# Optimization experiments

Hardware: AMD Instinct MI355X
Metric: run time of the kernel (lower is better)

Reference implementation:

```python
import jax, jax.numpy as jnp
import numpy as np

N, M, D = 16384, 1024, 32


def setup_inputs() -> dict:
    key = jax.random.key(0)
    k1, k2 = jax.random.split(key)
    x = jax.random.normal(k1, (N, D), dtype=jnp.float32)
    centers = jax.random.normal(k2, (M, D), dtype=jnp.float32)
    sigma = jnp.ones((M, D), dtype=jnp.float32)  # get_sigma_ones(s=1.0)
    return {"x": x, "centers": centers, "sigma": sigma}


def reference(x, centers, sigma):
    # Gaussian RBF kernel: exp(-0.5 * delta^T invCov delta) / sqrt((2pi)^D det(S))
    d = x.shape[1]
    s2 = sigma ** 2  # (M, D)
    # invCovMat: inverse of per-center diagonal covariance -> diag(1/s2)
    invCov = jnp.eye(d, dtype=x.dtype) * (1.0 / s2)[:, :, None]  # (M, D, D)
    # denom: sqrt((2pi)^D * prod(s2))
    k = (2.0 * np.pi) ** d  # python float, safe for D=32 in f32
    detS = jnp.sqrt(jnp.asarray(k, x.dtype) * jnp.prod(s2, axis=1))  # (M,)
    delta = x[:, None, :] - centers[None, :, :]  # (N, M, D)
    # batched (1,D) @ (D,D) per (n,m) pair, then elementwise * delta and reduce
    q = jnp.einsum('nmd,mde->nme', delta, invCov)  # (N, M, D)
    X = jnp.sum(q * delta, axis=2)  # (N, M) squared Mahalanobis distance
    return jnp.exp(-0.5 * X) / detS[None, :]  # (N, M)
```

## Files before the change

kernel.cpp:

```cpp
#include <hip/hip_runtime.h>


#define N_  16384
#define M_  1024
#define D_  32
#define NT  32
#define BLK 256

typedef float v4f __attribute__((ext_vector_type(4)));
#define PIN(v) asm volatile("" : "+v"(v))

__global__ __launch_bounds__(BLK, 6) void rbf_kernel(
    const float* __restrict__ x, const float* __restrict__ centers,
    const float* __restrict__ sigma, float* __restrict__ out)
{
    const int tid = threadIdx.x;
    const int m   = blockIdx.x * BLK + tid;
    const int n0  = blockIdx.y * NT;

    __shared__ __align__(16) float r2s[NT];

    {
        const v4f* xg = (const v4f*)(x + (size_t)n0 * D_);
        v4f v = xg[tid];
        float s = fmaf(v.x, v.x, fmaf(v.y, v.y, fmaf(v.z, v.z, v.w * v.w)));
        s += __shfl_xor(s, 1);
        s += __shfl_xor(s, 2);
        s += __shfl_xor(s, 4);
        if ((tid & 7) == 0) r2s[tid >> 3] = s;
    }
    __syncthreads();

    const float L2E      = 1.4426950408889634f;
    const float LOG2_2PI = 2.6514961294723187f;

    float s2_0 = 0.f, ld = 0.f;
    bool uf = true;
    {
        const float* sg = sigma + (size_t)m * D_;
        #pragma unroll
        for (int d = 0; d < D_; ++d) {
            float s  = sg[d];
            float s2 = s * s;
            if (d == 0) s2_0 = s2;
            uf = uf && (s2 == s2_0);
            ld += log2f(s2);
        }
    }

    if (__all((int)uf)) {
        const float w0 = 1.0f / s2_0;
        v4f A[D_ / 4];
        float b = 0.f;
        {
            const v4f* cg = (const v4f*)(centers + (size_t)m * D_);
            #pragma unroll
            for (int j = 0; j < D_ / 4; ++j) {
                v4f c = cg[j];
                v4f a = c * w0;
                A[j] = a;
                b = fmaf(c.x, a.x, b);
                b = fmaf(c.y, a.y, b);
                b = fmaf(c.z, a.z, b);
                b = fmaf(c.w, a.w, b);
            }
        }
        #pragma unroll
        for (int j = 0; j < D_ / 4; ++j) PIN(A[j]);

        const float c0 = fmaf(-0.5f * L2E, b, -0.5f * (D_ * LOG2_2PI + ld));
        const float qc = -0.5f * L2E * w0;

        const v4f* r2v = (const v4f*)r2s;
        float* o0 = out + (size_t)n0 * M_ + m;

        #pragma unroll 1
        for (int i = 0; i < NT; i += 8) {
            v4f ra = r2v[i / 4];
            v4f rb = r2v[i / 4 + 1];
            #pragma unroll
            for (int k = 0; k < 8; ++k) {
                const v4f* row = (const v4f*)(x + (size_t)(n0 + i + k) * D_);
                v4f x0 = row[0], x1 = row[1], x2 = row[2], x3 = row[3];
                v4f x4 = row[4], x5 = row[5], x6 = row[6], x7 = row[7];
                v4f p = x0 * A[0];
                v4f q = x1 * A[1];
                p += x2 * A[2];  q += x3 * A[3];
                p += x4 * A[4];  q += x5 * A[5];
                p += x6 * A[6];  q += x7 * A[7];
                v4f t = p + q;
                float dot = (t.x + t.y) + (t.z + t.w);
                float rr  = (k < 4) ? ra[k] : rb[k - 4];
                float f   = fmaf(L2E, dot, fmaf(qc, rr, c0));
                __builtin_nontemporal_store(__builtin_amdgcn_exp2f(f),
                                            o0 + (size_t)(i + k) * M_);
            }
        }
    } else {
        const float c0 = -0.5f * (D_ * LOG2_2PI + ld);
        const float* cg = centers + (size_t)m * D_;
        const float* sg = sigma   + (size_t)m * D_;
        #pragma unroll 1
        for (int i = 0; i < NT; ++i) {
            const float* xr = x + (size_t)(n0 + i) * D_;
            float a0 = 0.f, a1 = 0.f;
            #pragma unroll
            for (int d = 0; d < D_; d += 2) {
                float s0 = sg[d], s1 = sg[d + 1];
                float t0 = xr[d]     - cg[d];
                float t1 = xr[d + 1] - cg[d + 1];
                a0 = fmaf(t0 * (1.0f / (s0 * s0)), t0, a0);
                a1 = fmaf(t1 * (1.0f / (s1 * s1)), t1, a1);
            }
            float f = fmaf(-0.5f * L2E, a0 + a1, c0);
            out[(size_t)(n0 + i) * M_ + m] = __builtin_amdgcn_exp2f(f);
        }
    }
}

extern "C" void kernel_launch(void* const* d_in, const int* in_sizes, int n_in,
                              void* d_out, int out_size, void* d_ws, size_t ws_size,
                              hipStream_t stream) {
    const float* x = (const float*)d_in[0];
    const float* c = (const float*)d_in[1];
    const float* s = (const float*)d_in[2];
    float* out = (float*)d_out;
    dim3 grid(M_ / BLK, N_ / NT);
    rbf_kernel<<<grid, BLK, 0, stream>>>(x, c, s, out);
}
```

Measured before the change: 96.10 us.

## Precompute per-center RBF coefficients in a separate prologue kernel

Adds a small pre-kernel that computes, once per center, the scaled center vectors (stored transposed for coalesced loads), the log-determinant constant, the quadratic coefficient and a uniform-sigma flag, all written to workspace. The main kernel then loads these instead of having each of the 512 row-blocks recompute 32 log2f calls and a scaled center vector per thread. A fallback monolithic kernel runs when no workspace is available. The cost is an extra kernel launch and a dependency between the two kernels.

```diff
diff --git a/kernel.cpp b/kernel.cpp
--- a/kernel.cpp
+++ b/kernel.cpp
@@ -10,9 +10,65 @@
 typedef float v4f __attribute__((ext_vector_type(4)));
 #define PIN(v) asm volatile("" : "+v"(v))
 
-__global__ __launch_bounds__(BLK, 6) void rbf_kernel(
+#define L2E_      1.4426950408889634f
+#define LOG2_2PI_ 2.6514961294723187f
+
+#define WS_NEED (8 * M_ * 16 + 4 * M_ * 4)
+
+__global__ __launch_bounds__(64) void rbf_pre(
+    const float* __restrict__ centers, const float* __restrict__ sigma,
+    v4f* __restrict__ At, float* __restrict__ qc, float* __restrict__ c0f,
+    float* __restrict__ g0, float* __restrict__ flag)
+{
+    const int m = blockIdx.x * 64 + threadIdx.x;
+    const v4f* cg = (const v4f*)(centers + (size_t)m * D_);
+    const v4f* sg = (const v4f*)(sigma   + (size_t)m * D_);
+
+    v4f cv[8], s2v[8];
+    #pragma unroll
+    for (int j = 0; j < 8; ++j) {
+        cv[j] = cg[j];
+        v4f s = sg[j];
+        s2v[j] = s * s;
+    }
+    const float s2_0 = s2v[0].x;
+    bool uf = true;
+    float pr = 1.0f;
+    #pragma unroll
+    for (int j = 0; j < 8; ++j) {
+        #pragma unroll
+        for (int e = 0; e < 4; ++e) {
+            float v = s2v[j][e];
+            uf = uf && (v == s2_0);
+            pr *= v;
+        }
+    }
+    const float ld = log2f(pr);
+
+    const float w0 = 1.0f / s2_0;
+    float b = 0.f;
+    #pragma unroll
+    for (int j = 0; j < 8; ++j) {
+        v4f a = cv[j] * w0;
+        At[(size_t)j * M_ + m] = a;
+        b = fmaf(cv[j].x, a.x, b);
+        b = fmaf(cv[j].y, a.y, b);
+        b = fmaf(cv[j].z, a.z, b);
+        b = fmaf(cv[j].w, a.w, b);
+    }
+    const float g = -0.5f * (D_ * LOG2_2PI_ + ld);
+    g0[m]   = g;
+    c0f[m]  = fmaf(-0.5f * L2E_, b, g);
+    qc[m]   = -0.5f * L2E_ * w0;
+    flag[m] = uf ? 1.0f : 0.0f;
+}
+
+__global__ __launch_bounds__(BLK, 6) void rbf_main(
     const float* __restrict__ x, const float* __restrict__ centers,
-    const float* __restrict__ sigma, float* __restrict__ out)
+    const float* __restrict__ sigma, float* __restrict__ out,
+    const v4f* __restrict__ At, const float* __restrict__ qc,
+    const float* __restrict__ c0f, const float* __restrict__ g0,
+    const float* __restrict__ flag)
 {
     const int tid = threadIdx.x;
     const int m   = blockIdx.x * BLK + tid;
@@ -31,45 +87,15 @@
     }
     __syncthreads();
 
-    const float L2E      = 1.4426950408889634f;
-    const float LOG2_2PI = 2.6514961294723187f;
-
-    float s2_0 = 0.f, ld = 0.f;
-    bool uf = true;
-    {
-        const float* sg = sigma + (size_t)m * D_;
-        #pragma unroll
-        for (int d = 0; d < D_; ++d) {
-            float s  = sg[d];
-            float s2 = s * s;
-            if (d == 0) s2_0 = s2;
-            uf = uf && (s2 == s2_0);
-            ld += log2f(s2);
-        }
-    }
-
-    if (__all((int)uf)) {
-        const float w0 = 1.0f / s2_0;
-        v4f A[D_ / 4];
-        float b = 0.f;
-        {
-            const v4f* cg = (const v4f*)(centers + (size_t)m * D_);
-            #pragma unroll
-            for (int j = 0; j < D_ / 4; ++j) {
-                v4f c = cg[j];
-                v4f a = c * w0;
-                A[j] = a;
-                b = fmaf(c.x, a.x, b);
-                b = fmaf(c.y, a.y, b);
-                b = fmaf(c.z, a.z, b);
-                b = fmaf(c.w, a.w, b);
-            }
-        }
-        #pragma unroll
-        for (int j = 0; j < D_ / 4; ++j) PIN(A[j]);
-
-        const float c0 = fmaf(-0.5f * L2E, b, -0.5f * (D_ * LOG2_2PI + ld));
-        const float qc = -0.5f * L2E * w0;
+    const float fl = flag[m];
+    if (__all(fl != 0.0f)) {
+        const float qcm = qc[m];
+        const float c0m = c0f[m];
+        v4f A[8];
+        #pragma unroll
+        for (int j = 0; j < 8; ++j) A[j] = At[(size_t)j * M_ + m];
+        #pragma unroll
+        for (int j = 0; j < 8; ++j) PIN(A[j]);
 
         const v4f* r2v = (const v4f*)r2s;
         float* o0 = out + (size_t)n0 * M_ + m;
@@ -91,13 +117,13 @@
                 v4f t = p + q;
                 float dot = (t.x + t.y) + (t.z + t.w);
                 float rr  = (k < 4) ? ra[k] : rb[k - 4];
-                float f   = fmaf(L2E, dot, fmaf(qc, rr, c0));
+                float f   = fmaf(L2E_, dot, fmaf(qcm, rr, c0m));
                 __builtin_nontemporal_store(__builtin_amdgcn_exp2f(f),
                                             o0 + (size_t)(i + k) * M_);
             }
         }
     } else {
-        const float c0 = -0.5f * (D_ * LOG2_2PI + ld);
+        const float c0 = g0[m];
         const float* cg = centers + (size_t)m * D_;
         const float* sg = sigma   + (size_t)m * D_;
         #pragma unroll 1
@@ -112,7 +138,108 @@
                 a0 = fmaf(t0 * (1.0f / (s0 * s0)), t0, a0);
                 a1 = fmaf(t1 * (1.0f / (s1 * s1)), t1, a1);
             }
-            float f = fmaf(-0.5f * L2E, a0 + a1, c0);
+            float f = fmaf(-0.5f * L2E_, a0 + a1, c0);
+            out[(size_t)(n0 + i) * M_ + m] = __builtin_amdgcn_exp2f(f);
+        }
+    }
+}
+
+__global__ __launch_bounds__(BLK, 6) void rbf_mono(
+    const float* __restrict__ x, const float* __restrict__ centers,
+    const float* __restrict__ sigma, float* __restrict__ out)
+{
+    const int tid = threadIdx.x;
+    const int m   = blockIdx.x * BLK + tid;
+    const int n0  = blockIdx.y * NT;
+
+    __shared__ __align__(16) float r2s[NT];
+    {
+        const v4f* xg = (const v4f*)(x + (size_t)n0 * D_);
+        v4f v = xg[tid];
+        float s = fmaf(v.x, v.x, fmaf(v.y, v.y, fmaf(v.z, v.z, v.w * v.w)));
+        s += __shfl_xor(s, 1);
+        s += __shfl_xor(s, 2);
+        s += __shfl_xor(s, 4);
+        if ((tid & 7) == 0) r2s[tid >> 3] = s;
+    }
+    __syncthreads();
+
+    float s2_0 = 0.f, ld = 0.f;
+    bool uf = true;
+    {
+        const float* sg = sigma + (size_t)m * D_;
+        #pragma unroll
+        for (int d = 0; d < D_; ++d) {
+            float s  = sg[d];
+            float s2 = s * s;
+            if (d == 0) s2_0 = s2;
+            uf = uf && (s2 == s2_0);
+            ld += log2f(s2);
+        }
+    }
+
+    if (__all((int)uf)) {
+        const float w0 = 1.0f / s2_0;
+        v4f A[8];
+        float b = 0.f;
+        {
+            const v4f* cg = (const v4f*)(centers + (size_t)m * D_);
+            #pragma unroll
+            for (int j = 0; j < 8; ++j) {
+                v4f c = cg[j];
+                v4f a = c * w0;
+                A[j] = a;
+                b = fmaf(c.x, a.x, b); b = fmaf(c.y, a.y, b);
+                b = fmaf(c.z, a.z, b); b = fmaf(c.w, a.w, b);
+            }
+        }
+        #pragma unroll
+        for (int j = 0; j < 8; ++j) PIN(A[j]);
+
+        const float c0 = fmaf(-0.5f * L2E_, b, -0.5f * (D_ * LOG2_2PI_ + ld));
+        const float qc = -0.5f * L2E_ * w0;
+        const v4f* r2v = (const v4f*)r2s;
+        float* o0 = out + (size_t)n0 * M_ + m;
+
+        #pragma unroll 1
+        for (int i = 0; i < NT; i += 8) {
+            v4f ra = r2v[i / 4];
+            v4f rb = r2v[i / 4 + 1];
+            #pragma unroll
+            for (int k = 0; k < 8; ++k) {
+                const v4f* row = (const v4f*)(x + (size_t)(n0 + i + k) * D_);
+                v4f x0 = row[0], x1 = row[1], x2 = row[2], x3 = row[3];
+                v4f x4 = row[4], x5 = row[5], x6 = row[6], x7 = row[7];
+                v4f p = x0 * A[0];
+                v4f q = x1 * A[1];
+                p += x2 * A[2];  q += x3 * A[3];
+                p += x4 * A[4];  q += x5 * A[5];
+                p += x6 * A[6];  q += x7 * A[7];
+                v4f t = p + q;
+                float dot = (t.x + t.y) + (t.z + t.w);
+                float rr  = (k < 4) ? ra[k] : rb[k - 4];
+                float f   = fmaf(L2E_, dot, fmaf(qc, rr, c0));
+                __builtin_nontemporal_store(__builtin_amdgcn_exp2f(f),
+                                            o0 + (size_t)(i + k) * M_);
+            }
+        }
+    } else {
+        const float c0 = -0.5f * (D_ * LOG2_2PI_ + ld);
+        const float* cg = centers + (size_t)m * D_;
+        const float* sg = sigma   + (size_t)m * D_;
+        #pragma unroll 1
+        for (int i = 0; i < NT; ++i) {
+            const float* xr = x + (size_t)(n0 + i) * D_;
+            float a0 = 0.f, a1 = 0.f;
+            #pragma unroll
+            for (int d = 0; d < D_; d += 2) {
+                float s0 = sg[d], s1 = sg[d + 1];
+                float t0 = xr[d]     - cg[d];
+                float t1 = xr[d + 1] - cg[d + 1];
+                a0 = fmaf(t0 * (1.0f / (s0 * s0)), t0, a0);
+                a1 = fmaf(t1 * (1.0f / (s1 * s1)), t1, a1);
+            }
+            float f = fmaf(-0.5f * L2E_, a0 + a1, c0);
             out[(size_t)(n0 + i) * M_ + m] = __builtin_amdgcn_exp2f(f);
         }
     }
@@ -125,6 +252,19 @@
     const float* c = (const float*)d_in[1];
     const float* s = (const float*)d_in[2];
     float* out = (float*)d_out;
-    dim3 grid(M_ / BLK, N_ / NT);
-    rbf_kernel<<<grid, BLK, 0, stream>>>(x, c, s, out);
-}
+
+    if (ws_size >= (size_t)WS_NEED && d_ws != nullptr) {
+        char*  w    = (char*)d_ws;
+        v4f*   At   = (v4f*)w;
+        float* qc   = (float*)(w + 8 * M_ * 16);
+        float* c0f  = qc  + M_;
+        float* g0   = c0f + M_;
+        float* flag = g0  + M_;
+        rbf_pre<<<dim3(M_ / 64), 64, 0, stream>>>(c, s, At, qc, c0f, g0, flag);
+        dim3 grid(M_ / BLK, N_ / NT);
+        rbf_main<<<grid, BLK, 0, stream>>>(x, c, s, out, At, qc, c0f, g0, flag);
+    } else {
+        dim3 grid(M_ / BLK, N_ / NT);
+        rbf_mono<<<grid, BLK, 0, stream>>>(x, c, s, out);
+    }
+}
```

Result: faster. 90.42 us (median of 2 runs) (-5.9%).
